# Performance work log

Hardware: AMD Instinct MI355X
Metric: run time of the kernel (lower is better)

Reference implementation:

```python
import jax, jax.numpy as jnp
import numpy as np

R = 10  # num_relations
NUM_GRAPHS = 64


def rgcn_layer(x, W, root, b, src, dst, etype):
    # x: [N, Din], W: [R, Din, H], root: [Din, H], b: [H]
    N = x.shape[0]
    H = W.shape[-1]
    # per-relation transform of all nodes: [R, N, H]
    h_all = jnp.einsum('nd,rdh->rnh', x, W)
    # gather transformed source features per edge by its relation: [E, H]
    msg = h_all[etype, src]
    # mean-aggregate per (dst, relation) pair, then sum over relations (PyG RGCNConv semantics)
    key = dst * R + etype
    sums = jax.ops.segment_sum(msg, key, num_segments=N * R)  # [N*R, H]
    cnt = jax.ops.segment_sum(jnp.ones((etype.shape[0],), x.dtype), key, num_segments=N * R)
    agg = (sums.reshape(N, R, H) / jnp.clip(cnt.reshape(N, R, 1), 1.0, None)).sum(axis=1)
    return agg + x @ root + b


def setup_inputs() -> dict:
    key = jax.random.key(0)
    ks = jax.random.split(key, 12)
    N, E, DIN, H = 100000, 3200000, 128, 64
    x = jax.random.normal(ks[0], (N, DIN), dtype=jnp.float32)
    edge_index = jax.random.randint(ks[1], (2, E), 0, N, dtype=jnp.int64)
    edge_type = jax.random.randint(ks[2], (E,), 0, R, dtype=jnp.int64)
    batch = jnp.sort(jax.random.randint(ks[3], (N,), 0, NUM_GRAPHS, dtype=jnp.int64))
    s1 = 1.0 / np.sqrt(DIN)
    s2 = 1.0 / np.sqrt(H)
    W1 = jax.random.uniform(ks[4], (R, DIN, H), jnp.float32, -s1, s1)
    root1 = jax.random.uniform(ks[5], (DIN, H), jnp.float32, -s1, s1)
    b1 = jnp.zeros((H,), jnp.float32)
    W2 = jax.random.uniform(ks[6], (R, H, H), jnp.float32, -s2, s2)
    root2 = jax.random.uniform(ks[7], (H, H), jnp.float32, -s2, s2)
    b2 = jnp.zeros((H,), jnp.float32)
    cls_w = jax.random.uniform(ks[8], (H, 1), jnp.float32, -s2, s2)
    cls_b = jnp.zeros((1,), jnp.float32)
    return {"x": x, "edge_index": edge_index, "edge_type": edge_type, "batch": batch,
            "W1": W1, "root1": root1, "b1": b1, "W2": W2, "root2": root2, "b2": b2,
            "cls_w": cls_w, "cls_b": cls_b}


def reference(x, edge_index, edge_type, batch, W1, root1, b1, W2, root2, b2, cls_w, cls_b):
    src, dst = edge_index[0], edge_index[1]
    h = jax.nn.relu(rgcn_layer(x, W1, root1, b1, src, dst, edge_type))   # dropout = identity (eval)
    h = jax.nn.relu(rgcn_layer(h, W2, root2, b2, src, dst, edge_type))
    # global mean pool per graph
    sums = jax.ops.segment_sum(h, batch, num_segments=NUM_GRAPHS)        # [G, H]
    cnt = jax.ops.segment_sum(jnp.ones((h.shape[0],), h.dtype), batch, num_segments=NUM_GRAPHS)
    pooled = sums / jnp.clip(cnt[:, None], 1.0, None)
    out = pooled @ cls_w + cls_b                                          # [G, 1]
    return out.reshape(-1)
```

## Files before the change

### kernel.cpp

```cpp
#include <hip/hip_runtime.h>

#define R_REL 10
#define HD 64
#define BSH 8
#define KPB (256 * R_REL)
#define SORT_CAP 12288

typedef __attribute__((ext_vector_type(8))) short short8;
typedef __attribute__((ext_vector_type(4))) float floatx4;
typedef __attribute__((ext_vector_type(8))) unsigned short ushort8;

__device__ inline unsigned short f32_to_bf16_rne(float f) {
    unsigned int u = __float_as_uint(f);
    unsigned int r = (u + 0x7FFFu + ((u >> 16) & 1u)) >> 16;
    return (unsigned short)r;
}
__device__ inline float bf16_to_f32(unsigned short h) {
    return __uint_as_float(((unsigned int)h) << 16);
}
__device__ inline float bf16lo(unsigned int u) { return __uint_as_float(u << 16); }
__device__ inline float bf16hi(unsigned int u) { return __uint_as_float(u & 0xFFFF0000u); }

__device__ __forceinline__ void gload_lds16(const unsigned short* g, unsigned short* l) {
    __builtin_amdgcn_global_load_lds(
        (const __attribute__((address_space(1))) unsigned int*)g,
        (__attribute__((address_space(3))) unsigned int*)l, 16, 0, 0);
}

#define BAR_VMCNT(N)                                              \
    do {                                                          \
        asm volatile("s_waitcnt vmcnt(" #N ")" ::: "memory");     \
        __builtin_amdgcn_sched_barrier(0);                        \
        __builtin_amdgcn_s_barrier();                             \
        __builtin_amdgcn_sched_barrier(0);                        \
    } while (0)

__global__ __launch_bounds__(256) void bhist_kernel(const int* __restrict__ dst,
                                                    int* __restrict__ bcnt, int E) {
    __shared__ int l[512];
    int t = threadIdx.x;
    l[t] = 0; l[t + 256] = 0;
    __syncthreads();
    int e0 = blockIdx.x * 4096;
    for (int i = t; i < 4096; i += 256) {
        int e = e0 + i;
        if (e < E) atomicAdd(&l[dst[e] >> BSH], 1);
    }
    __syncthreads();
    if (l[t]) atomicAdd(&bcnt[t], l[t]);
    if (l[t + 256]) atomicAdd(&bcnt[t + 256], l[t + 256]);
}

__global__ void bscan_kernel(const int* __restrict__ bcnt, int* __restrict__ boff,
                             int* __restrict__ gcursor, int NBK, int E) {
    int t = threadIdx.x;
    int v = (t < NBK) ? bcnt[t] : 0;
    __shared__ int tmp[512];
    tmp[t] = v;
    __syncthreads();
    for (int off = 1; off < 512; off <<= 1) {
        int u = (t >= off) ? tmp[t - off] : 0;
        __syncthreads();
        tmp[t] += u;
        __syncthreads();
    }
    int excl = tmp[t] - v;
    if (t < NBK) { boff[t] = excl; gcursor[t] = excl; }
    if (t == 0) boff[NBK] = E;
}

__global__ __launch_bounds__(256) void bscatter_kernel(const int* __restrict__ src,
                                                       const int* __restrict__ dst,
                                                       const int* __restrict__ et,
                                                       int* __restrict__ gcursor,
                                                       unsigned int* __restrict__ staged,
                                                       int E) {
    __shared__ int lcnt[512];
    __shared__ int lstart[512];
    __shared__ int lbase[512];
    __shared__ int tmp[256];
    __shared__ unsigned int lbuf[4096];
    __shared__ unsigned short lbkt[4096];
    int t = threadIdx.x;
    int e0 = blockIdx.x * 4096;
    int nthis = min(4096, E - e0);
    lcnt[t] = 0; lcnt[t + 256] = 0;
    __syncthreads();
    for (int i = t; i < nthis; i += 256) atomicAdd(&lcnt[dst[e0 + i] >> BSH], 1);
    __syncthreads();
    int c0 = lcnt[2 * t], c1 = lcnt[2 * t + 1];
    int ps = c0 + c1;
    tmp[t] = ps;
    __syncthreads();
    for (int off = 1; off < 256; off <<= 1) {
        int u = (t >= off) ? tmp[t - off] : 0;
        __syncthreads();
        tmp[t] += u;
        __syncthreads();
    }
    int ex = tmp[t] - ps;
    lstart[2 * t] = ex; lstart[2 * t + 1] = ex + c0;
    lbase[2 * t]     = (c0 > 0) ? atomicAdd(&gcursor[2 * t], c0) : 0;
    lbase[2 * t + 1] = (c1 > 0) ? atomicAdd(&gcursor[2 * t + 1], c1) : 0;
    __syncthreads();
    lcnt[t] = 0; lcnt[t + 256] = 0;
    __syncthreads();
    for (int i = t; i < nthis; i += 256) {
        int dd = dst[e0 + i];
        int bk = dd >> BSH;
        int lk = (dd & ((1 << BSH) - 1)) * R_REL + et[e0 + i];
        unsigned int p = ((unsigned int)lk << 17) | (unsigned int)src[e0 + i];
        int pos = lstart[bk] + atomicAdd(&lcnt[bk], 1);
        lbuf[pos] = p; lbkt[pos] = (unsigned short)bk;
    }
    __syncthreads();
    for (int i = t; i < nthis; i += 256) {
        int bk = lbkt[i];
        staged[lbase[bk] + i - lstart[bk]] = lbuf[i];
    }
}

__global__ __launch_bounds__(256) void sortfill_kernel(const unsigned int* __restrict__ staged,
                                                       const int* __restrict__ boff,
                                                       int* __restrict__ dcnt,
                                                       int2* __restrict__ edata,
                                                       int N, int Ntot) {
    __shared__ int hist[KPB];
    __shared__ float wkey[KPB];
    __shared__ int part[256];
    __shared__ int lsrc[SORT_CAP];
    __shared__ unsigned short lkey[SORT_CAP];
    int t = threadIdx.x, b = blockIdx.x;
    int s0 = boff[b], s1 = boff[b + 1];
#pragma unroll
    for (int j = 0; j < KPB / 256; ++j) hist[t + j * 256] = 0;
    __syncthreads();
    for (int i = s0 + t; i < s1; i += 256)
        atomicAdd(&hist[staged[i] >> 17], 1);
    __syncthreads();
    int base = t * (KPB / 256);
    int c[KPB / 256];
    int s = 0;
#pragma unroll
    for (int j = 0; j < KPB / 256; ++j) {
        c[j] = hist[base + j]; s += c[j];
        wkey[base + j] = 1.0f / fmaxf((float)c[j], 1.0f);
    }
    int dglob = b * 256 + t;
    if (dglob < Ntot) dcnt[dglob] = s;
    part[t] = s;
    __syncthreads();
    for (int off = 1; off < 256; off <<= 1) {
        int u = (t >= off) ? part[t - off] : 0;
        __syncthreads();
        part[t] += u;
        __syncthreads();
    }
    int run = part[t] - s;
#pragma unroll
    for (int j = 0; j < KPB / 256; ++j) { hist[base + j] = run; run += c[j]; }
    __syncthreads();
    for (int i = s0 + t; i < s1; i += 256) {
        unsigned int p = staged[i];
        int lk = p >> 17;
        int pos = atomicAdd(&hist[lk], 1);
        if (pos < SORT_CAP) { lsrc[pos] = (int)(p & 0x1FFFFu); lkey[pos] = (unsigned short)lk; }
        else {
            int rel = lk % R_REL;
            edata[s0 + pos] = make_int2(rel * N + (int)(p & 0x1FFFFu), __float_as_int(wkey[lk]));
        }
    }
    __syncthreads();
    int m = min(s1 - s0, SORT_CAP);
    for (int j = t; j < m; j += 256) {
        int lk = lkey[j];
        int rel = lk % R_REL;
        edata[s0 + j] = make_int2(rel * N + lsrc[j], __float_as_int(wkey[lk]));
    }
}

__global__ void scan1_kernel(const int* __restrict__ cnt, int* __restrict__ bsum, int M) {
    int b = blockIdx.x, tid = threadIdx.x;
    int base = b * 1024 + tid * 4;
    int s = 0;
#pragma unroll
    for (int j = 0; j < 4; ++j) { int i = base + j; if (i < M) s += cnt[i]; }
    for (int off = 32; off > 0; off >>= 1) s += __shfl_down(s, off);
    __shared__ int wsum[4];
    int lane = tid & 63, wid = tid >> 6;
    if (lane == 0) wsum[wid] = s;
    __syncthreads();
    if (tid == 0) bsum[b] = wsum[0] + wsum[1] + wsum[2] + wsum[3];
}

__global__ void scan2_kernel(const int* __restrict__ bsum, int* __restrict__ boff, int NB) {
    int tid = threadIdx.x;
    int lane = tid & 63, wid = tid >> 6;
    int v = (tid < NB) ? bsum[tid] : 0;
    int x = v;
    for (int off = 1; off < 64; off <<= 1) { int u = __shfl_up(x, off); if (lane >= off) x += u; }
    __shared__ int wsum[16];
    if (lane == 63) wsum[wid] = x;
    __syncthreads();
    int woff = 0;
    for (int w = 0; w < wid; ++w) woff += wsum[w];
    if (tid < NB) boff[tid] = x + woff - v;
}

__global__ void scan3_kernel(const int* __restrict__ cnt, const int* __restrict__ boff,
                             int* __restrict__ rowptr, int M) {
    int b = blockIdx.x, tid = threadIdx.x;
    int base = b * 1024 + tid * 4;
    int c[4]; int s = 0;
#pragma unroll
    for (int j = 0; j < 4; ++j) { int i = base + j; c[j] = (i < M) ? cnt[i] : 0; s += c[j]; }
    int lane = tid & 63, wid = tid >> 6;
    int x = s;
    for (int off = 1; off < 64; off <<= 1) { int u = __shfl_up(x, off); if (lane >= off) x += u; }
    __shared__ int wsum[4];
    if (lane == 63) wsum[wid] = x;
    __syncthreads();
    int woff = 0;
    for (int w = 0; w < wid; ++w) woff += wsum[w];
    int run = boff[b] + x + woff - s;
#pragma unroll
    for (int j = 0; j < 4; ++j) {
        int i = base + j;
        if (i < M) {
            rowptr[i] = run; run += c[j];
            if (i == M - 1) rowptr[M] = run;
        }
    }
}

__global__ void split_kernel(const float* __restrict__ src, unsigned short* __restrict__ hi,
                             unsigned short* __restrict__ lo, int n) {
    int i = blockIdx.x * 256 + threadIdx.x;
    if (i < n) {
        float v = src[i];
        unsigned short h = f32_to_bf16_rne(v);
        hi[i] = h;
        lo[i] = f32_to_bf16_rne(v - bf16_to_f32(h));
    }
}

__global__ void wsplit_kernel(const float* __restrict__ W, const float* __restrict__ root,
                              unsigned short* __restrict__ hi, int K) {
    int idx = blockIdx.x * 256 + threadIdx.x;
    int total = (R_REL + 1) * HD * K;
    if (idx >= total) return;
    int rel = idx / (HD * K);
    int rem = idx - rel * HD * K;
    int n = rem / K, k = rem - n * K;
    float v = (rel < R_REL) ? W[((size_t)rel * K + k) * HD + n] : root[(size_t)k * HD + n];
    int ks = k ^ ((n & 7) << 3);
    hi[rel * HD * K + n * K + ks] = f32_to_bf16_rne(v);
}

template <int K>
__global__ __launch_bounds__(256, 5)
void gemm_mfma(const unsigned short* __restrict__ Xhi,
               const unsigned short* __restrict__ Xlo,
               const unsigned short* __restrict__ Wthi,
               unsigned short* __restrict__ hout,
               float* __restrict__ fout, int N) {
    constexpr int NS = K / 32;
    constexpr int TILE_SH = HD * K;
    __shared__ unsigned short wlds[2 * TILE_SH];
    const int tid = threadIdx.x;
    const int w = tid >> 6, lane = tid & 63;
    const int quad = lane >> 4, l16 = lane & 15;
    const int wr = w >> 1, wc = w & 1;
    const int n0 = blockIdx.x * 64;
    const int nodeA = n0 + wc * 32 + l16;
    const int nodeB = nodeA + 16;
    const bool vA = nodeA < N, vB = nodeB < N;
    const bool full = (n0 + 64 <= N);

    short8 Xh[2][NS], Xl[2][NS];
#pragma unroll
    for (int s = 0; s < NS; ++s) {
        short8 z;
#pragma unroll
        for (int q = 0; q < 8; ++q) z[q] = 0;
        Xh[0][s] = z; Xl[0][s] = z; Xh[1][s] = z; Xl[1][s] = z;
        if (vA) {
            Xh[0][s] = *(const short8*)(Xhi + (size_t)nodeA * K + s * 32 + quad * 8);
            Xl[0][s] = *(const short8*)(Xlo + (size_t)nodeA * K + s * 32 + quad * 8);
        }
        if (vB) {
            Xh[1][s] = *(const short8*)(Xhi + (size_t)nodeB * K + s * 32 + quad * 8);
            Xl[1][s] = *(const short8*)(Xlo + (size_t)nodeB * K + s * 32 + quad * 8);
        }
    }

    auto stage = [&](int rel, int b) {
        const unsigned short* hsrc = Wthi + (size_t)rel * TILE_SH;
        unsigned short* dst0 = wlds + b * TILE_SH;
#pragma unroll
        for (int j = 0; j < NS; ++j) {
            int q = j * 4 + w;
            gload_lds16(hsrc + q * 512 + lane * 8, dst0 + q * 512);
        }
    };

    stage(0, 0);
    BAR_VMCNT(0);

    const int swzb = (l16 & 7) << 4;
    const size_t NHD = (size_t)N * HD;

#pragma unroll
    for (int c = 0; c <= R_REL; ++c) {
        const int cur = c & 1;
        if (c < R_REL) stage(c + 1, cur ^ 1);
        const char* wb = (const char*)(wlds + cur * TILE_SH);
        floatx4 acc[2][2];
#pragma unroll
        for (int mt = 0; mt < 2; ++mt) {
            floatx4 z = {0.f, 0.f, 0.f, 0.f};
            acc[mt][0] = z; acc[mt][1] = z;
        }
#pragma unroll
        for (int s = 0; s < NS; ++s) {
            const int koffb = ((s * 32 + quad * 8) * 2) ^ swzb;
#pragma unroll
            for (int mt = 0; mt < 2; ++mt) {
                const int rowb = (wr * 32 + mt * 16 + l16) * (K * 2);
                short8 Wh = *(const short8*)(wb + rowb + koffb);
#pragma unroll
                for (int nh = 0; nh < 2; ++nh) {
                    acc[mt][nh] = __builtin_amdgcn_mfma_f32_16x16x32_bf16(Wh, Xh[nh][s], acc[mt][nh], 0, 0, 0);
                    acc[mt][nh] = __builtin_amdgcn_mfma_f32_16x16x32_bf16(Wh, Xl[nh][s], acc[mt][nh], 0, 0, 0);
                }
            }
        }
        if (c < R_REL) {
#pragma unroll
            for (int mt = 0; mt < 2; ++mt) {
#pragma unroll
                for (int nh = 0; nh < 2; ++nh) {
                    int node = (nh == 0) ? nodeA : nodeB;
                    if (nh == 0 ? vA : vB) {
                        unsigned int d0 = (unsigned int)f32_to_bf16_rne(acc[mt][nh][0]) |
                                          ((unsigned int)f32_to_bf16_rne(acc[mt][nh][1]) << 16);
                        unsigned int d1 = (unsigned int)f32_to_bf16_rne(acc[mt][nh][2]) |
                                          ((unsigned int)f32_to_bf16_rne(acc[mt][nh][3]) << 16);
                        *(uint2*)(hout + (size_t)c * NHD + (size_t)node * HD +
                                  wr * 32 + mt * 16 + quad * 4) = make_uint2(d0, d1);
                    }
                }
            }
        } else {
#pragma unroll
            for (int mt = 0; mt < 2; ++mt) {
#pragma unroll
                for (int nh = 0; nh < 2; ++nh) {
                    int node = (nh == 0) ? nodeA : nodeB;
                    if (nh == 0 ? vA : vB)
                        *(floatx4*)(fout + (size_t)node * HD + wr * 32 + mt * 16 + quad * 4) =
                            acc[mt][nh];
                }
            }
        }
        if (c < R_REL) {
            if (full) BAR_VMCNT(4); else BAR_VMCNT(0);
        }
    }
}

__global__ __launch_bounds__(256) void agg_kernel(const unsigned short* __restrict__ hc,
                                                  const int* __restrict__ rowptr,
                                                  const int2* __restrict__ edata,
                                                  float* __restrict__ acc, int N) {
    int gid = blockIdx.x * 256 + threadIdx.x;
    int d = gid >> 6;
    if (d >= N) return;
    int lane = threadIdx.x & 63;
    int quarter = lane >> 4, l16 = lane & 15;
    int e0 = rowptr[d], e1 = rowptr[d + 1];
    int ne = e1 - e0;
    if (ne == 0) return;
    float s0 = 0.f, s1 = 0.f, s2 = 0.f, s3 = 0.f;
    for (int rb = 0; rb < ne; rb += 64) {
        int nthis = min(64, ne - rb);
        int2 ed = make_int2(0, 0);
        if (lane < nthis) ed = edata[e0 + rb + lane];
        int off = ed.x << 6;
        float wv = __int_as_float(ed.y);
        for (int j = 0; j < nthis; j += 8) {
            int   oa = __shfl(off, j + quarter);
            float wa = __shfl(wv,  j + quarter);
            int   ob = __shfl(off, j + 4 + quarter);
            float wb = __shfl(wv,  j + 4 + quarter);
            uint2 da = *(const uint2*)(hc + oa + l16 * 4);
            uint2 db = *(const uint2*)(hc + ob + l16 * 4);
            s0 += wa * bf16lo(da.x); s1 += wa * bf16hi(da.x);
            s2 += wa * bf16lo(da.y); s3 += wa * bf16hi(da.y);
            s0 += wb * bf16lo(db.x); s1 += wb * bf16hi(db.x);
            s2 += wb * bf16lo(db.y); s3 += wb * bf16hi(db.y);
        }
    }
    s0 += __shfl_xor(s0, 16); s1 += __shfl_xor(s1, 16);
    s2 += __shfl_xor(s2, 16); s3 += __shfl_xor(s3, 16);
    s0 += __shfl_xor(s0, 32); s1 += __shfl_xor(s1, 32);
    s2 += __shfl_xor(s2, 32); s3 += __shfl_xor(s3, 32);
    if (lane < 16) {
        float4* ap = (float4*)(acc + (size_t)d * HD + l16 * 4);
        float4 a = *ap;
        a.x += s0; a.y += s1; a.z += s2; a.w += s3;
        *ap = a;
    }
}

__global__ void fin1_kernel(const float* __restrict__ acc, const float* __restrict__ bias,
                            unsigned short* __restrict__ hi, unsigned short* __restrict__ lo,
                            int NH) {
    int i = blockIdx.x * 256 + threadIdx.x;
    if (i < NH) {
        float v = fmaxf(acc[i] + bias[i & (HD - 1)], 0.f);
        unsigned short h = f32_to_bf16_rne(v);
        hi[i] = h;
        lo[i] = f32_to_bf16_rne(v - bf16_to_f32(h));
    }
}

__global__ __launch_bounds__(256) void pool_kernel(const float* __restrict__ acc,
                                                   const float* __restrict__ bias,
                                                   const int* __restrict__ batch,
                                                   float* __restrict__ pooled,
                                                   float* __restrict__ gcnt, int N) {
    int w = blockIdx.x * 4 + (threadIdx.x >> 6);
    int lane = threadIdx.x & 63;
    int base = w * 64;
    if (base >= N) return;
    int nn = min(64, N - base);
    float b = bias[lane];
    int g_l = (base + lane < N) ? batch[base + lane] : -1;
    int g_first = __shfl(g_l, 0);
    int g_last = __shfl(g_l, nn - 1);
    if (nn == 64 && g_first == g_last) {
        float p0 = 0.f, p1 = 0.f, p2 = 0.f, p3 = 0.f;
#pragma unroll
        for (int i = 0; i < 64; i += 4) {
            p0 += fmaxf(acc[(size_t)(base + i + 0) * HD + lane] + b, 0.f);
            p1 += fmaxf(acc[(size_t)(base + i + 1) * HD + lane] + b, 0.f);
            p2 += fmaxf(acc[(size_t)(base + i + 2) * HD + lane] + b, 0.f);
            p3 += fmaxf(acc[(size_t)(base + i + 3) * HD + lane] + b, 0.f);
        }
        atomicAdd(&pooled[g_first * HD + lane], (p0 + p1) + (p2 + p3));
        if (lane == 0) atomicAdd(&gcnt[g_first], 64.f);
    } else {
        int cur = g_first; float s = 0.f; int cnt = 0;
        for (int i = 0; i < nn; ++i) {
            int g = __shfl(g_l, i);
            if (g != cur) {
                atomicAdd(&pooled[cur * HD + lane], s);
                if (lane == 0) atomicAdd(&gcnt[cur], (float)cnt);
                cur = g; s = 0.f; cnt = 0;
            }
            s += fmaxf(acc[(size_t)(base + i) * HD + lane] + b, 0.f);
            cnt++;
        }
        atomicAdd(&pooled[cur * HD + lane], s);
        if (lane == 0) atomicAdd(&gcnt[cur], (float)cnt);
    }
}

__global__ void cls_kernel(const float* __restrict__ pooled, const float* __restrict__ gcnt,
                           const float* __restrict__ cls_w, const float* __restrict__ cls_b,
                           float* __restrict__ out) {
    int g = threadIdx.x;
    float invc = 1.0f / fmaxf(gcnt[g], 1.0f);
    float acc = 0.f;
    for (int j = 0; j < 64; ++j) acc += pooled[g * 64 + j] * cls_w[j];
    out[g] = acc * invc + cls_b[0];
}

extern "C" void kernel_launch(void* const* d_in, const int* in_sizes, int n_in,
                              void* d_out, int out_size, void* d_ws, size_t ws_size,
                              hipStream_t stream) {
    const float* x     = (const float*)d_in[0];
    const int*   eidx  = (const int*)d_in[1];
    const int*   et    = (const int*)d_in[2];
    const int*   batch = (const int*)d_in[3];
    const float* W1    = (const float*)d_in[4];
    const float* root1 = (const float*)d_in[5];
    const float* b1    = (const float*)d_in[6];
    const float* W2    = (const float*)d_in[7];
    const float* root2 = (const float*)d_in[8];
    const float* b2    = (const float*)d_in[9];
    const float* cls_w = (const float*)d_in[10];
    const float* cls_b = (const float*)d_in[11];

    const int N = in_sizes[3];
    const int E = in_sizes[2];
    const int NB = (N + 1023) / 1024;
    const int NBK = (N + (1 << BSH) - 1) >> BSH;
    const int* srcp = eidx;
    const int* dstp = eidx + E;

    char* ws = (char*)d_ws;
    size_t off = 0;
    auto alloc = [&](size_t bytes) -> void* {
        void* p = ws + off;
        off = (off + bytes + 255) & ~(size_t)255;
        return p;
    };
    unsigned short* Xhi  = (unsigned short*)alloc((size_t)N * 128 * 2);
    unsigned short* Xlo  = (unsigned short*)alloc((size_t)N * 128 * 2);
    float*          accb = (float*)alloc((size_t)N * HD * 4);
    unsigned short* Wt1hi = (unsigned short*)alloc((size_t)(R_REL + 1) * HD * 128 * 2);
    unsigned short* Wt2hi = (unsigned short*)alloc((size_t)(R_REL + 1) * HD * HD * 2);
    int2*  edata  = (int2*)alloc((size_t)E * 8);
    int*   rowptr = (int*)alloc((size_t)(N + 1) * 4);
    int*   dcnt   = (int*)alloc((size_t)N * 4);
    int*   bsum   = (int*)alloc((size_t)NB * 4);
    int*   bofs   = (int*)alloc((size_t)NB * 4);
    int*   bcnt   = (int*)alloc(512 * 4);
    int*   bboff  = (int*)alloc(513 * 4);
    int*   gcur   = (int*)alloc(512 * 4);
    float* pooled = (float*)alloc((size_t)(64 * HD + 64) * 4);
    float* gcnt   = pooled + 64 * HD;
    unsigned short* h_chunk = (unsigned short*)alloc((size_t)R_REL * N * HD * 2);

    unsigned int* staged = (unsigned int*)Xhi;
    unsigned short* H1hi = Xhi;
    unsigned short* H1lo = Xlo;

    hipMemsetAsync(bcnt, 0, 512 * 4, stream);
    hipMemsetAsync(pooled, 0, (size_t)(64 * HD + 64) * 4, stream);

    int nchunks = (E + 4095) / 4096;
    bhist_kernel<<<nchunks, 256, 0, stream>>>(dstp, bcnt, E);
    bscan_kernel<<<1, 512, 0, stream>>>(bcnt, bboff, gcur, NBK, E);
    bscatter_kernel<<<nchunks, 256, 0, stream>>>(srcp, dstp, et, gcur, staged, E);
    sortfill_kernel<<<NBK, 256, 0, stream>>>(staged, bboff, dcnt, edata, N, N);
    scan1_kernel<<<NB, 256, 0, stream>>>(dcnt, bsum, N);
    scan2_kernel<<<1, 1024, 0, stream>>>(bsum, bofs, NB);
    scan3_kernel<<<NB, 256, 0, stream>>>(dcnt, bofs, rowptr, N);

    int NK = N * 128;
    split_kernel<<<(NK + 255) / 256, 256, 0, stream>>>(x, Xhi, Xlo, NK);
    int tw1 = (R_REL + 1) * HD * 128, tw2 = (R_REL + 1) * HD * HD;
    wsplit_kernel<<<(tw1 + 255) / 256, 256, 0, stream>>>(W1, root1, Wt1hi, 128);
    wsplit_kernel<<<(tw2 + 255) / 256, 256, 0, stream>>>(W2, root2, Wt2hi, HD);

    const int gemmBlocks = (N + 63) / 64;
    const int aggBlocks  = (int)(((size_t)N * 64 + 255) / 256);
    const int NH = N * HD;

    gemm_mfma<128><<<gemmBlocks, 256, 0, stream>>>(Xhi, Xlo, Wt1hi, h_chunk, accb, N);
    agg_kernel<<<aggBlocks, 256, 0, stream>>>(h_chunk, rowptr, edata, accb, N);
    fin1_kernel<<<(NH + 255) / 256, 256, 0, stream>>>(accb, b1, H1hi, H1lo, NH);

    gemm_mfma<64><<<gemmBlocks, 256, 0, stream>>>(H1hi, H1lo, Wt2hi, h_chunk, accb, N);
    agg_kernel<<<aggBlocks, 256, 0, stream>>>(h_chunk, rowptr, edata, accb, N);

    int poolWaves = (N + 63) / 64;
    pool_kernel<<<(poolWaves + 3) / 4, 256, 0, stream>>>(accb, b2, batch, pooled, gcnt, N);
    cls_kernel<<<1, 64, 0, stream>>>(pooled, gcnt, cls_w, cls_b, (float*)d_out);
}
```

Baseline: 600.8 us.

## Use 512-thread GEMM blocks with each wave owning 16 nodes across all 64 outputs

The per-relation GEMM goes from 256-thread blocks covering 64 nodes to 512-thread blocks covering 128 nodes. Each wave now handles 16 nodes against all four 16-column output tiles, instead of a 2x2 split of nodes and columns. This halves how many blocks stage the shared weight tile into LDS per node, and each wave writes a full contiguous 64-wide output row. In exchange, each wave reads the whole weight tile from LDS per node group and holds fewer X registers, with a changed occupancy target.

```diff
diff --git a/kernel.cpp b/kernel.cpp
--- a/kernel.cpp
+++ b/kernel.cpp
@@ -258,7 +258,7 @@
 }
 
 template <int K>
-__global__ __launch_bounds__(256, 5)
+__global__ __launch_bounds__(512, 6)
 void gemm_mfma(const unsigned short* __restrict__ Xhi,
                const unsigned short* __restrict__ Xlo,
                const unsigned short* __restrict__ Wthi,
@@ -266,31 +266,26 @@
                float* __restrict__ fout, int N) {
     constexpr int NS = K / 32;
     constexpr int TILE_SH = HD * K;
+    constexpr int SC = K / 64;
     __shared__ unsigned short wlds[2 * TILE_SH];
     const int tid = threadIdx.x;
     const int w = tid >> 6, lane = tid & 63;
     const int quad = lane >> 4, l16 = lane & 15;
-    const int wr = w >> 1, wc = w & 1;
-    const int n0 = blockIdx.x * 64;
-    const int nodeA = n0 + wc * 32 + l16;
-    const int nodeB = nodeA + 16;
-    const bool vA = nodeA < N, vB = nodeB < N;
-    const bool full = (n0 + 64 <= N);
-
-    short8 Xh[2][NS], Xl[2][NS];
+    const int n0 = blockIdx.x * 128;
+    const int node = n0 + w * 16 + l16;
+    const bool valid = node < N;
+    const bool full = (n0 + 128 <= N);
+
+    short8 Xh[NS], Xl[NS];
 #pragma unroll
     for (int s = 0; s < NS; ++s) {
         short8 z;
 #pragma unroll
         for (int q = 0; q < 8; ++q) z[q] = 0;
-        Xh[0][s] = z; Xl[0][s] = z; Xh[1][s] = z; Xl[1][s] = z;
-        if (vA) {
-            Xh[0][s] = *(const short8*)(Xhi + (size_t)nodeA * K + s * 32 + quad * 8);
-            Xl[0][s] = *(const short8*)(Xlo + (size_t)nodeA * K + s * 32 + quad * 8);
-        }
-        if (vB) {
-            Xh[1][s] = *(const short8*)(Xhi + (size_t)nodeB * K + s * 32 + quad * 8);
-            Xl[1][s] = *(const short8*)(Xlo + (size_t)nodeB * K + s * 32 + quad * 8);
+        Xh[s] = z; Xl[s] = z;
+        if (valid) {
+            Xh[s] = *(const short8*)(Xhi + (size_t)node * K + s * 32 + quad * 8);
+            Xl[s] = *(const short8*)(Xlo + (size_t)node * K + s * 32 + quad * 8);
         }
     }
 
@@ -298,8 +293,8 @@
         const unsigned short* hsrc = Wthi + (size_t)rel * TILE_SH;
         unsigned short* dst0 = wlds + b * TILE_SH;
 #pragma unroll
-        for (int j = 0; j < NS; ++j) {
-            int q = j * 4 + w;
+        for (int j = 0; j < SC; ++j) {
+            int q = j * 8 + w;
             gload_lds16(hsrc + q * 512 + lane * 8, dst0 + q * 512);
         }
     };
@@ -315,52 +310,38 @@
         const int cur = c & 1;
         if (c < R_REL) stage(c + 1, cur ^ 1);
         const char* wb = (const char*)(wlds + cur * TILE_SH);
-        floatx4 acc[2][2];
-#pragma unroll
-        for (int mt = 0; mt < 2; ++mt) {
-            floatx4 z = {0.f, 0.f, 0.f, 0.f};
-            acc[mt][0] = z; acc[mt][1] = z;
-        }
+        floatx4 acc[4];
+#pragma unroll
+        for (int mt = 0; mt < 4; ++mt) { floatx4 z = {0.f, 0.f, 0.f, 0.f}; acc[mt] = z; }
 #pragma unroll
         for (int s = 0; s < NS; ++s) {
             const int koffb = ((s * 32 + quad * 8) * 2) ^ swzb;
 #pragma unroll
-            for (int mt = 0; mt < 2; ++mt) {
-                const int rowb = (wr * 32 + mt * 16 + l16) * (K * 2);
+            for (int mt = 0; mt < 4; ++mt) {
+                const int rowb = (mt * 16 + l16) * (K * 2);
                 short8 Wh = *(const short8*)(wb + rowb + koffb);
-#pragma unroll
-                for (int nh = 0; nh < 2; ++nh) {
-                    acc[mt][nh] = __builtin_amdgcn_mfma_f32_16x16x32_bf16(Wh, Xh[nh][s], acc[mt][nh], 0, 0, 0);
-                    acc[mt][nh] = __builtin_amdgcn_mfma_f32_16x16x32_bf16(Wh, Xl[nh][s], acc[mt][nh], 0, 0, 0);
-                }
+                acc[mt] = __builtin_amdgcn_mfma_f32_16x16x32_bf16(Wh, Xh[s], acc[mt], 0, 0, 0);
+                acc[mt] = __builtin_amdgcn_mfma_f32_16x16x32_bf16(Wh, Xl[s], acc[mt], 0, 0, 0);
             }
         }
         if (c < R_REL) {
-#pragma unroll
-            for (int mt = 0; mt < 2; ++mt) {
-#pragma unroll
-                for (int nh = 0; nh < 2; ++nh) {
-                    int node = (nh == 0) ? nodeA : nodeB;
-                    if (nh == 0 ? vA : vB) {
-                        unsigned int d0 = (unsigned int)f32_to_bf16_rne(acc[mt][nh][0]) |
-                                          ((unsigned int)f32_to_bf16_rne(acc[mt][nh][1]) << 16);
-                        unsigned int d1 = (unsigned int)f32_to_bf16_rne(acc[mt][nh][2]) |
-                                          ((unsigned int)f32_to_bf16_rne(acc[mt][nh][3]) << 16);
-                        *(uint2*)(hout + (size_t)c * NHD + (size_t)node * HD +
-                                  wr * 32 + mt * 16 + quad * 4) = make_uint2(d0, d1);
-                    }
+            if (valid) {
+                unsigned short* hp = hout + (size_t)c * NHD + (size_t)node * HD;
+#pragma unroll
+                for (int mt = 0; mt < 4; ++mt) {
+                    unsigned int d0 = (unsigned int)f32_to_bf16_rne(acc[mt][0]) |
+                                      ((unsigned int)f32_to_bf16_rne(acc[mt][1]) << 16);
+                    unsigned int d1 = (unsigned int)f32_to_bf16_rne(acc[mt][2]) |
+                                      ((unsigned int)f32_to_bf16_rne(acc[mt][3]) << 16);
+                    *(uint2*)(hp + mt * 16 + quad * 4) = make_uint2(d0, d1);
                 }
             }
         } else {
-#pragma unroll
-            for (int mt = 0; mt < 2; ++mt) {
-#pragma unroll
-                for (int nh = 0; nh < 2; ++nh) {
-                    int node = (nh == 0) ? nodeA : nodeB;
-                    if (nh == 0 ? vA : vB)
-                        *(floatx4*)(fout + (size_t)node * HD + wr * 32 + mt * 16 + quad * 4) =
-                            acc[mt][nh];
-                }
+            if (valid) {
+                float* fp = fout + (size_t)node * HD;
+#pragma unroll
+                for (int mt = 0; mt < 4; ++mt)
+                    *(floatx4*)(fp + mt * 16 + quad * 4) = acc[mt];
             }
         }
         if (c < R_REL) {
@@ -546,15 +527,15 @@
     wsplit_kernel<<<(tw1 + 255) / 256, 256, 0, stream>>>(W1, root1, Wt1hi, 128);
     wsplit_kernel<<<(tw2 + 255) / 256, 256, 0, stream>>>(W2, root2, Wt2hi, HD);
 
-    const int gemmBlocks = (N + 63) / 64;
+    const int gemmBlocks = (N + 127) / 128;
     const int aggBlocks  = (int)(((size_t)N * 64 + 255) / 256);
     const int NH = N * HD;
 
-    gemm_mfma<128><<<gemmBlocks, 256, 0, stream>>>(Xhi, Xlo, Wt1hi, h_chunk, accb, N);
+    gemm_mfma<128><<<gemmBlocks, 512, 0, stream>>>(Xhi, Xlo, Wt1hi, h_chunk, accb, N);
     agg_kernel<<<aggBlocks, 256, 0, stream>>>(h_chunk, rowptr, edata, accb, N);
     fin1_kernel<<<(NH + 255) / 256, 256, 0, stream>>>(accb, b1, H1hi, H1lo, NH);
 
-    gemm_mfma<64><<<gemmBlocks, 256, 0, stream>>>(H1hi, H1lo, Wt2hi, h_chunk, accb, N);
+    gemm_mfma<64><<<gemmBlocks, 512, 0, stream>>>(H1hi, H1lo, Wt2hi, h_chunk, accb, N);
     agg_kernel<<<aggBlocks, 256, 0, stream>>>(h_chunk, rowptr, edata, accb, N);
 
     int poolWaves = (N + 63) / 64;
```

After: 570.2 us. -5.1%, faster.
